# Performance work log

Measured on AMD Instinct MI355X. Metric: run time of the kernel, lower is better.

## Reference

```python
import jax, jax.numpy as jnp
import numpy as np

C = 768; NH = 12; HD = C // NH; P = 16; IMG = 256; HS = IMG // P  # 16x16 patch grid
WIN = 7; HWP = WIN // 2  # half window (pad)
DEPTH = 12; MLP = 4 * C
B = 32; T = 1
OFFS = [(dh, dw) for dh in range(WIN) for dw in range(WIN)]


def ln(x, g, b, eps=1e-5):
    mu = jnp.mean(x, axis=-1, keepdims=True)
    var = jnp.mean((x - mu) ** 2, axis=-1, keepdims=True)
    return (x - mu) * jax.lax.rsqrt(var + eps) * g + b


def local_attn(x, qkv_w, proj_w, proj_b):
    # x: (B, N, C) with N = HS*HS (T=1); sliding-window attention, zero-padded keys
    Bc, N, _ = x.shape
    qkv = (x @ qkv_w.T).reshape(Bc, N, 3, NH, HD)
    q, k, v = [jnp.transpose(qkv[:, :, i], (0, 2, 1, 3)).reshape(Bc, NH, HS, HS, HD)
               for i in range(3)]
    scale = HD ** -0.5
    kp = jnp.pad(k, ((0, 0), (0, 0), (HWP, HWP), (HWP, HWP), (0, 0)))
    vp = jnp.pad(v, ((0, 0), (0, 0), (HWP, HWP), (HWP, HWP), (0, 0)))
    # per-offset logits; padded (zero) keys give logit 0, matching torch's zero-pad softmax
    scores = jnp.stack([
        jnp.einsum('bnhwd,bnhwd->bnhw', q, kp[:, :, dh:dh + HS, dw:dw + HS]) * scale
        for dh, dw in OFFS], axis=-1)  # (B, NH, HS, HS, 49)
    attn = jax.nn.softmax(scores, axis=-1)
    out = sum(attn[..., i, None] * vp[:, :, dh:dh + HS, dw:dw + HS]
              for i, (dh, dw) in enumerate(OFFS))  # (B, NH, HS, HS, HD)
    out = jnp.transpose(out, (0, 2, 3, 1, 4)).reshape(Bc, N, C)
    return out @ proj_w.T + proj_b


def global_attn(x, in_w, in_b, out_w, out_b):
    Bc, N, _ = x.shape
    qkv = x @ in_w.T + in_b
    q, k, v = jnp.split(qkv, 3, axis=-1)
    hds = lambda t: t.reshape(Bc, N, NH, HD).transpose(0, 2, 1, 3)
    q, k, v = hds(q), hds(k), hds(v)
    s = jnp.einsum('bnqd,bnkd->bnqk', q, k) * (HD ** -0.5)
    a = jax.nn.softmax(s, axis=-1)
    o = jnp.einsum('bnqk,bnkd->bnqd', a, v).transpose(0, 2, 1, 3).reshape(Bc, N, C)
    return o @ out_w.T + out_b


def setup_inputs() -> dict:
    key = jax.random.key(0)
    ks = iter(jax.random.split(key, 40))
    s = 0.02
    inp = {
        'x': jax.random.normal(next(ks), (B, T, 3, IMG, IMG), jnp.float32),
        'aspect_ratio': jax.random.uniform(next(ks), (B,), jnp.float32),
        'conv_w': jax.random.normal(next(ks), (C, 3, P, P), jnp.float32) * s,
        'conv_b': jnp.zeros((C,), jnp.float32),
        'pe_g': jnp.ones((C,), jnp.float32), 'pe_b': jnp.zeros((C,), jnp.float32),
        'ar_token': jax.random.normal(next(ks), (1, 1, C), jnp.float32) * s,
        'pos_embed': jax.random.normal(next(ks), (1, 100 * HS * HS + 1, C), jnp.float32) * s,
        'ln1_g': jnp.ones((DEPTH, C), jnp.float32), 'ln1_b': jnp.zeros((DEPTH, C), jnp.float32),
        'ln2_g': jnp.ones((DEPTH, C), jnp.float32), 'ln2_b': jnp.zeros((DEPTH, C), jnp.float32),
        'loc_qkv_w': jax.random.normal(next(ks), (6, 3 * C, C), jnp.float32) * s,
        'loc_proj_w': jax.random.normal(next(ks), (6, C, C), jnp.float32) * s,
        'loc_proj_b': jnp.zeros((6, C), jnp.float32),
        'glob_in_w': jax.random.normal(next(ks), (6, 3 * C, C), jnp.float32) * s,
        'glob_in_b': jnp.zeros((6, 3 * C), jnp.float32),
        'glob_out_w': jax.random.normal(next(ks), (6, C, C), jnp.float32) * s,
        'glob_out_b': jnp.zeros((6, C), jnp.float32),
        'mlp_w1': jax.random.normal(next(ks), (DEPTH, MLP, C), jnp.float32) * s,
        'mlp_b1': jnp.zeros((DEPTH, MLP), jnp.float32),
        'mlp_w2': jax.random.normal(next(ks), (DEPTH, C, MLP), jnp.float32) * s,
        'mlp_b2': jnp.zeros((DEPTH, C), jnp.float32),
        'fin_g': jnp.ones((C,), jnp.float32), 'fin_b': jnp.zeros((C,), jnp.float32),
    }
    return inp


def reference(x, aspect_ratio, conv_w, conv_b, pe_g, pe_b, ar_token, pos_embed,
              ln1_g, ln1_b, ln2_g, ln2_b,
              loc_qkv_w, loc_proj_w, loc_proj_b,
              glob_in_w, glob_in_b, glob_out_w, glob_out_b,
              mlp_w1, mlp_b1, mlp_w2, mlp_b2, fin_g, fin_b):
    Bc, Tc, Ci, Hi, Wi = x.shape
    # patch embed: non-overlapping conv == block reshape + einsum
    xf = x.reshape(Bc * Tc, Ci, HS, P, HS, P)
    patches = jnp.einsum('bchpwq,ecpq->bhwe', xf, conv_w) + conv_b
    patches = patches.reshape(Bc, Tc * HS * HS, C)
    patches = ln(patches, pe_g, pe_b)
    # aspect ratio token
    ar = ar_token * (1.0 + aspect_ratio[:, None, None] * 0.1)  # (B,1,C)
    h = jnp.concatenate([patches, ar], axis=1)
    h = h + pos_embed[:, :h.shape[1], :]
    for i in range(DEPTH):
        if i % 2 == 0:  # local attention block (AR token stripped, N == HS*HS+1)
            li = i // 2
            tok, art = h[:, :-1], h[:, -1:]
            tok = tok + local_attn(ln(tok, ln1_g[i], ln1_b[i]),
                                   loc_qkv_w[li], loc_proj_w[li], loc_proj_b[li])
            h = jnp.concatenate([tok, art], axis=1)
        else:
            gi = i // 2
            h = h + global_attn(ln(h, ln1_g[i], ln1_b[i]),
                                glob_in_w[gi], glob_in_b[gi], glob_out_w[gi], glob_out_b[gi])
        m = ln(h, ln2_g[i], ln2_b[i])
        m = jax.nn.gelu(m @ mlp_w1[i].T + mlp_b1[i], approximate=False)
        h = h + m @ mlp_w2[i].T + mlp_b2[i]
    return ln(h, fin_g, fin_b)
```

## Files before the change

### kernel.cpp

```cpp
#include <hip/hip_runtime.h>
#include <cmath>

#define NHEADS 12
#define NTOK   257
#define BATCH  32
#define ROWS   (BATCH*NTOK)
#define PROWS  (BATCH*256)
#define GTPAD  288

typedef __attribute__((ext_vector_type(8))) short short8;
typedef __attribute__((ext_vector_type(8))) unsigned short u16x8;
typedef __attribute__((ext_vector_type(4))) float f32x4;

__device__ __forceinline__ unsigned short f2bf(float f) {
    unsigned u = __float_as_uint(f);
    unsigned r = (u + 0x7FFFu + ((u >> 16) & 1u)) >> 16;
    return (unsigned short)r;
}
__device__ __forceinline__ float b2f(unsigned short us) {
    return __uint_as_float((unsigned)us << 16);
}
__device__ __forceinline__ void gload16(const void* g, void* l) {
    __builtin_amdgcn_global_load_lds(
        (const __attribute__((address_space(1))) void*)g,
        (__attribute__((address_space(3))) void*)l, 16, 0, 0);
}

template<bool BIAS, bool GELU, bool RES, bool SKIPAR, bool OUTBF>
__global__ __launch_bounds__(256) void gemm_bf16(
    const unsigned short* __restrict__ A, const unsigned short* __restrict__ W,
    const float* __restrict__ bias, void* __restrict__ outv,
    int M, int N, int K)
{
    __shared__ unsigned short As[128 * 32];
    __shared__ unsigned short Bs[128 * 32];
    const int tid = threadIdx.x;
    const int lane = tid & 63, wid = tid >> 6;
    const int wr = wid >> 1, wc = wid & 1;
    const int bm = blockIdx.y * 128, bn = blockIdx.x * 128;

    f32x4 acc[4][4];
    #pragma unroll
    for (int i = 0; i < 4; i++)
        #pragma unroll
        for (int j = 0; j < 4; j++) acc[i][j] = (f32x4)0.f;

    const int srow = lane >> 2;
    const int skk  = (lane & 3) * 8;
    const int l15  = lane & 15;
    const int lg   = lane >> 4;

    for (int k0 = 0; k0 < K; k0 += 32) {
        #pragma unroll
        for (int cc = 0; cc < 2; cc++) {
            int c = 2 * wid + cc;
            int row = c * 16 + srow;
            gload16(A + (size_t)(bm + row) * K + k0 + skk, &As[c * 512]);
            gload16(W + (size_t)(bn + row) * K + k0 + skk, &Bs[c * 512]);
        }
        __syncthreads();
        short8 af[4], bf[4];
        #pragma unroll
        for (int i = 0; i < 4; i++)
            af[i] = *(const short8*)&As[(wr * 64 + i * 16 + l15) * 32 + lg * 8];
        #pragma unroll
        for (int j = 0; j < 4; j++)
            bf[j] = *(const short8*)&Bs[(wc * 64 + j * 16 + l15) * 32 + lg * 8];
        #pragma unroll
        for (int i = 0; i < 4; i++)
            #pragma unroll
            for (int j = 0; j < 4; j++)
                acc[i][j] = __builtin_amdgcn_mfma_f32_16x16x32_bf16(af[i], bf[j], acc[i][j], 0, 0, 0);
        __syncthreads();
    }

    float bcol[4];
    #pragma unroll
    for (int j = 0; j < 4; j++)
        bcol[j] = BIAS ? bias[bn + wc * 64 + j * 16 + l15] : 0.f;

    #pragma unroll
    for (int i = 0; i < 4; i++) {
        #pragma unroll
        for (int r = 0; r < 4; r++) {
            int row = bm + wr * 64 + i * 16 + lg * 4 + r;
            if (row >= M) continue;
            if (SKIPAR && (row % NTOK) == (NTOK - 1)) continue;
            #pragma unroll
            for (int j = 0; j < 4; j++) {
                int col = bn + wc * 64 + j * 16 + l15;
                float v = acc[i][j][r] + bcol[j];
                if (GELU) v = 0.5f * v * (1.0f + erff(v * 0.70710678118654752f));
                size_t idx = (size_t)row * N + col;
                if (OUTBF) {
                    ((unsigned short*)outv)[idx] = f2bf(v);
                } else {
                    float* o = (float*)outv;
                    if (RES) o[idx] += v; else o[idx] = v;
                }
            }
        }
    }
}

template<bool OUTBF>
__global__ __launch_bounds__(256) void ln_kernel(
    const float* __restrict__ in, void* __restrict__ outv,
    const float* __restrict__ g, const float* __restrict__ bparm, int rows)
{
    int gw = blockIdx.x * 4 + (threadIdx.x >> 6);
    int lane = threadIdx.x & 63;
    if (gw >= rows) return;
    const float* x = in + (size_t)gw * 768;
    float4 v[3];
    #pragma unroll
    for (int i = 0; i < 3; i++) v[i] = *(const float4*)(x + i * 256 + lane * 4);
    float s = 0.f;
    #pragma unroll
    for (int i = 0; i < 3; i++) s += v[i].x + v[i].y + v[i].z + v[i].w;
    #pragma unroll
    for (int off = 32; off >= 1; off >>= 1) s += __shfl_xor(s, off, 64);
    float mu = s * (1.f / 768.f);
    float q = 0.f;
    #pragma unroll
    for (int i = 0; i < 3; i++) {
        float dx = v[i].x - mu, dy = v[i].y - mu, dz = v[i].z - mu, dw = v[i].w - mu;
        q += dx * dx + dy * dy + dz * dz + dw * dw;
    }
    #pragma unroll
    for (int off = 32; off >= 1; off >>= 1) q += __shfl_xor(q, off, 64);
    float rstd = rsqrtf(q * (1.f / 768.f) + 1e-5f);
    #pragma unroll
    for (int i = 0; i < 3; i++) {
        float4 gg = *(const float4*)(g + i * 256 + lane * 4);
        float4 bb = *(const float4*)(bparm + i * 256 + lane * 4);
        float rx = (v[i].x - mu) * rstd * gg.x + bb.x;
        float ry = (v[i].y - mu) * rstd * gg.y + bb.y;
        float rz = (v[i].z - mu) * rstd * gg.z + bb.z;
        float rw = (v[i].w - mu) * rstd * gg.w + bb.w;
        if (OUTBF) {
            ushort4 u;
            u.x = f2bf(rx); u.y = f2bf(ry); u.z = f2bf(rz); u.w = f2bf(rw);
            *(ushort4*)((unsigned short*)outv + (size_t)gw * 768 + i * 256 + lane * 4) = u;
        } else {
            *(float4*)((float*)outv + (size_t)gw * 768 + i * 256 + lane * 4) =
                make_float4(rx, ry, rz, rw);
        }
    }
}

__global__ __launch_bounds__(256) void f2b_kernel(
    const float* __restrict__ in, unsigned short* __restrict__ out, int n4)
{
    int i = blockIdx.x * 256 + threadIdx.x;
    if (i >= n4) return;
    float4 v = ((const float4*)in)[i];
    ushort4 u;
    u.x = f2bf(v.x); u.y = f2bf(v.y); u.z = f2bf(v.z); u.w = f2bf(v.w);
    ((ushort4*)out)[i] = u;
}

__global__ __launch_bounds__(256) void gather_patches(
    const float* __restrict__ x, unsigned short* __restrict__ A)
{
    int row = blockIdx.x;
    int b = row >> 8;
    int pp = row & 255;
    int ph = pp >> 4, pw = pp & 15;
    const float* xb = x + (size_t)b * 196608;
    for (int e = threadIdx.x; e < 768; e += 256) {
        int c = e >> 8;
        int r = e & 255;
        int p = r >> 4, q = r & 15;
        A[(size_t)row * 768 + e] = f2bf(xb[(size_t)c * 65536 + (ph * 16 + p) * 256 + pw * 16 + q]);
    }
}

__global__ __launch_bounds__(256) void build_h_kernel(
    const unsigned short* __restrict__ lnp, const float* __restrict__ pos,
    const float* __restrict__ artok, const float* __restrict__ aspect,
    float* __restrict__ h)
{
    int row = blockIdx.x;
    int b = row / NTOK;
    int t = row - b * NTOK;
    float* hp = h + (size_t)row * 768;
    int e = threadIdx.x;
    if (t < 256) {
        const unsigned short* lp = lnp + ((size_t)b * 256 + t) * 768;
        const float* pp = pos + (size_t)t * 768;
        #pragma unroll
        for (int i = 0; i < 3; i++) { int c = e + i * 256; hp[c] = b2f(lp[c]) + pp[c]; }
    } else {
        float f = 1.0f + aspect[b] * 0.1f;
        const float* pp = pos + (size_t)256 * 768;
        #pragma unroll
        for (int i = 0; i < 3; i++) { int c = e + i * 256; hp[c] = artok[c] * f + pp[c]; }
    }
}

__global__ __launch_bounds__(256) void transpose_v(
    const unsigned short* __restrict__ qkv, unsigned short* __restrict__ vt)
{
    __shared__ unsigned short T[64][72];
    const int bh = blockIdx.x;
    const int b = bh / NHEADS, nh = bh % NHEADS;
    const unsigned short* vbase = qkv + (size_t)b * NTOK * 2304 + 1536 + nh * 64;
    unsigned short* obase = vt + (size_t)bh * 64 * GTPAD;
    const int tid = threadIdx.x;

    for (int t0 = 0; t0 < GTPAD; t0 += 64) {
        #pragma unroll
        for (int rnd = 0; rnd < 2; rnd++) {
            int tl = rnd * 32 + (tid >> 3);
            int d0 = (tid & 7) * 8;
            int tok = t0 + tl;
            u16x8 v;
            if (tok < NTOK) {
                v = *(const u16x8*)(vbase + (size_t)tok * 2304 + d0);
            } else {
                #pragma unroll
                for (int i = 0; i < 8; i++) v[i] = 0;
            }
            #pragma unroll
            for (int i = 0; i < 8; i++) T[d0 + i][tl] = v[i];
        }
        __syncthreads();
        int d = tid >> 2, ts = (tid & 3) * 16;
        if (t0 + ts < GTPAD) {
            u16x8 o0, o1;
            #pragma unroll
            for (int i = 0; i < 8; i++) { o0[i] = T[d][ts + i]; o1[i] = T[d][ts + 8 + i]; }
            *(u16x8*)(obase + (size_t)d * GTPAD + t0 + ts) = o0;
            *(u16x8*)(obase + (size_t)d * GTPAD + t0 + ts + 8) = o1;
        }
        __syncthreads();
    }
}

__global__ __launch_bounds__(256) void local_attn_mfma(
    const unsigned short* __restrict__ qkv, const unsigned short* __restrict__ vt,
    unsigned short* __restrict__ out)
{
    __shared__ unsigned short P[4][16 * 136];
    const int wid = threadIdx.x >> 6, lane = threadIdx.x & 63;
    const int gw = blockIdx.x * 4 + wid;
    const int bh = gw >> 4, h0 = gw & 15;
    const int b = bh / NHEADS, nh = bh % NHEADS;
    const int l15 = lane & 15, lg = lane >> 4;
    const unsigned short* base = qkv + (size_t)b * NTOK * 2304 + nh * 64;
    const unsigned short* vtb = vt + (size_t)bh * 64 * GTPAD;
    unsigned short* Pw = P[wid];

    const int qtok = h0 * 16 + l15;
    short8 qf0 = *(const short8*)(base + (size_t)qtok * 2304 + lg * 8);
    short8 qf1 = *(const short8*)(base + (size_t)qtok * 2304 + 32 + lg * 8);

    int r0 = h0 - 3; r0 = r0 < 0 ? 0 : (r0 > 8 ? 8 : r0);

    f32x4 s[8];
    #pragma unroll
    for (int i = 0; i < 8; i++) {
        const unsigned short* kr = base + (size_t)((r0 + i) * 16 + l15) * 2304 + 768;
        short8 kf0 = *(const short8*)(kr + lg * 8);
        short8 kf1 = *(const short8*)(kr + 32 + lg * 8);
        f32x4 z = (f32x4)0.f;
        z = __builtin_amdgcn_mfma_f32_16x16x32_bf16(kf0, qf0, z, 0, 0, 0);
        z = __builtin_amdgcn_mfma_f32_16x16x32_bf16(kf1, qf1, z, 0, 0, 0);
        s[i] = z;
    }

    const int vlo = l15 - 3 < 0 ? 0 : l15 - 3;
    const int vhi = l15 + 3 > 15 ? 15 : l15 + 3;
    const int rlo = h0 - 3 < 0 ? 0 : h0 - 3;
    const int rhi = h0 + 3 > 15 ? 15 : h0 + 3;
    const int n_oob = 49 - (rhi - rlo + 1) * (vhi - vlo + 1);
    float m = n_oob > 0 ? 0.f : -1e30f;
    float sv[32];
    #pragma unroll
    for (int i = 0; i < 8; i++) {
        int kh = r0 + i;
        bool rowok = (kh >= rlo) && (kh <= rhi);
        #pragma unroll
        for (int r = 0; r < 4; r++) {
            int kw = lg * 4 + r;
            bool ok = rowok && (kw >= vlo) && (kw <= vhi);
            float xx = ok ? s[i][r] * 0.125f : -1e30f;
            sv[i * 4 + r] = xx;
            m = fmaxf(m, xx);
        }
    }
    m = fmaxf(m, __shfl_xor(m, 16, 64));
    m = fmaxf(m, __shfl_xor(m, 32, 64));
    float tsum = 0.f;
    #pragma unroll
    for (int i = 0; i < 8; i++) {
        float p0 = __expf(sv[i * 4 + 0] - m);
        float p1 = __expf(sv[i * 4 + 1] - m);
        float p2 = __expf(sv[i * 4 + 2] - m);
        float p3 = __expf(sv[i * 4 + 3] - m);
        tsum += p0 + p1 + p2 + p3;
        unsigned u0 = (unsigned)f2bf(p0) | ((unsigned)f2bf(p1) << 16);
        unsigned u1 = (unsigned)f2bf(p2) | ((unsigned)f2bf(p3) << 16);
        *(uint2*)((char*)Pw + l15 * 272 + i * 32 + lg * 8) = make_uint2(u0, u1);
    }
    tsum += __shfl_xor(tsum, 16, 64);
    tsum += __shfl_xor(tsum, 32, 64);
    float denom = tsum + (float)n_oob * __expf(-m);
    __syncthreads();

    f32x4 acc[4];
    #pragma unroll
    for (int d = 0; d < 4; d++) acc[d] = (f32x4)0.f;
    #pragma unroll
    for (int kt = 0; kt < 128; kt += 32) {
        short8 pf = *(const short8*)((char*)Pw + l15 * 272 + kt * 2 + lg * 16);
        #pragma unroll
        for (int d = 0; d < 4; d++) {
            short8 vf = *(const short8*)(vtb + (size_t)(d * 16 + l15) * GTPAD + r0 * 16 + kt + lg * 8);
            acc[d] = __builtin_amdgcn_mfma_f32_16x16x32_bf16(vf, pf, acc[d], 0, 0, 0);
        }
    }

    float inv = 1.f / denom;
    unsigned short* op = out + ((size_t)b * NTOK + qtok) * 768 + nh * 64;
    #pragma unroll
    for (int d = 0; d < 4; d++) {
        ushort4 o;
        o.x = f2bf(acc[d][0] * inv);
        o.y = f2bf(acc[d][1] * inv);
        o.z = f2bf(acc[d][2] * inv);
        o.w = f2bf(acc[d][3] * inv);
        *(ushort4*)(op + d * 16 + lg * 4) = o;
    }
}

__global__ __launch_bounds__(64) void global_attn_mfma(
    const unsigned short* __restrict__ qkv, const unsigned short* __restrict__ vt,
    unsigned short* __restrict__ out)
{
    __shared__ uint4 Pbuf[80];
    unsigned short* P = (unsigned short*)Pbuf;
    const int blk = blockIdx.x;
    const int bh = blk / 17, qt = blk % 17;
    const int b = bh / NHEADS, nh = bh % NHEADS;
    const int lane = threadIdx.x;
    const int l15 = lane & 15, lg = lane >> 4;
    const unsigned short* base = qkv + (size_t)b * NTOK * 2304 + nh * 64;
    const unsigned short* vtb = vt + (size_t)bh * 64 * GTPAD;

    int qrow = qt * 16 + l15;
    const bool qvalid = qrow < NTOK;
    if (!qvalid) qrow = NTOK - 1;
    short8 qf[2];
    qf[0] = *(const short8*)(base + (size_t)qrow * 2304 + lg * 8);
    qf[1] = *(const short8*)(base + (size_t)qrow * 2304 + 32 + lg * 8);

    f32x4 acc[4];
    #pragma unroll
    for (int i = 0; i < 4; i++) acc[i] = (f32x4)0.f;
    float m = -1e30f, l = 0.f;

    for (int kt = 0; kt < GTPAD; kt += 32) {
        f32x4 s[2];
        #pragma unroll
        for (int hh = 0; hh < 2; hh++) {
            int krow = kt + hh * 16 + l15;
            if (krow > NTOK - 1) krow = NTOK - 1;
            short8 kf0 = *(const short8*)(base + (size_t)krow * 2304 + 768 + lg * 8);
            short8 kf1 = *(const short8*)(base + (size_t)krow * 2304 + 768 + 32 + lg * 8);
            f32x4 z = (f32x4)0.f;
            z = __builtin_amdgcn_mfma_f32_16x16x32_bf16(kf0, qf[0], z, 0, 0, 0);
            z = __builtin_amdgcn_mfma_f32_16x16x32_bf16(kf1, qf[1], z, 0, 0, 0);
            s[hh] = z;
        }
        float sv[8];
        float mt = -1e30f;
        #pragma unroll
        for (int hh = 0; hh < 2; hh++)
            #pragma unroll
            for (int r = 0; r < 4; r++) {
                int key = kt + hh * 16 + lg * 4 + r;
                float v = s[hh][r] * 0.125f;
                if (key >= NTOK) v = -1e30f;
                sv[hh * 4 + r] = v;
                mt = fmaxf(mt, v);
            }
        mt = fmaxf(mt, __shfl_xor(mt, 16, 64));
        mt = fmaxf(mt, __shfl_xor(mt, 32, 64));
        float mn = fmaxf(m, mt);
        float cf = __expf(m - mn);
        float tsum = 0.f;
        unsigned short pb[8];
        #pragma unroll
        for (int i = 0; i < 8; i++) {
            float p = __expf(sv[i] - mn);
            tsum += p;
            pb[i] = f2bf(p);
        }
        tsum += __shfl_xor(tsum, 16, 64);
        tsum += __shfl_xor(tsum, 32, 64);
        l = l * cf + tsum;
        m = mn;
        #pragma unroll
        for (int i = 0; i < 4; i++) acc[i] *= cf;

        unsigned u0 = (unsigned)pb[0] | ((unsigned)pb[1] << 16);
        unsigned u1 = (unsigned)pb[2] | ((unsigned)pb[3] << 16);
        unsigned u2 = (unsigned)pb[4] | ((unsigned)pb[5] << 16);
        unsigned u3 = (unsigned)pb[6] | ((unsigned)pb[7] << 16);
        *(uint2*)((char*)P + l15 * 80 + lg * 8)      = make_uint2(u0, u1);
        *(uint2*)((char*)P + l15 * 80 + 32 + lg * 8) = make_uint2(u2, u3);
        __syncthreads();
        short8 pf = *(const short8*)((char*)P + l15 * 80 + lg * 16);
        #pragma unroll
        for (int d = 0; d < 4; d++) {
            short8 vf = *(const short8*)(vtb + (size_t)(d * 16 + l15) * GTPAD + kt + lg * 8);
            acc[d] = __builtin_amdgcn_mfma_f32_16x16x32_bf16(vf, pf, acc[d], 0, 0, 0);
        }
        __syncthreads();
    }

    if (qvalid) {
        float inv = 1.f / l;
        unsigned short* op = out + ((size_t)b * NTOK + qrow) * 768 + nh * 64;
        #pragma unroll
        for (int d = 0; d < 4; d++) {
            ushort4 o;
            o.x = f2bf(acc[d][0] * inv);
            o.y = f2bf(acc[d][1] * inv);
            o.z = f2bf(acc[d][2] * inv);
            o.w = f2bf(acc[d][3] * inv);
            *(ushort4*)(op + d * 16 + lg * 4) = o;
        }
    }
}

extern "C" void kernel_launch(void* const* d_in, const int* in_sizes, int n_in,
                              void* d_out, int out_size, void* d_ws, size_t ws_size,
                              hipStream_t stream)
{
    const float* x       = (const float*)d_in[0];
    const float* aspect  = (const float*)d_in[1];
    const float* conv_w  = (const float*)d_in[2];
    const float* conv_b  = (const float*)d_in[3];
    const float* pe_g    = (const float*)d_in[4];
    const float* pe_b    = (const float*)d_in[5];
    const float* ar_tok  = (const float*)d_in[6];
    const float* pos     = (const float*)d_in[7];
    const float* ln1_g   = (const float*)d_in[8];
    const float* ln1_b   = (const float*)d_in[9];
    const float* ln2_g   = (const float*)d_in[10];
    const float* ln2_b   = (const float*)d_in[11];
    const float* loc_qkv_w  = (const float*)d_in[12];
    const float* loc_proj_w = (const float*)d_in[13];
    const float* loc_proj_b = (const float*)d_in[14];
    const float* glob_in_w  = (const float*)d_in[15];
    const float* glob_in_b  = (const float*)d_in[16];
    const float* glob_out_w = (const float*)d_in[17];
    const float* glob_out_b = (const float*)d_in[18];
    const float* mlp_w1  = (const float*)d_in[19];
    const float* mlp_b1  = (const float*)d_in[20];
    const float* mlp_w2  = (const float*)d_in[21];
    const float* mlp_b2  = (const float*)d_in[22];
    const float* fin_g   = (const float*)d_in[23];
    const float* fin_b   = (const float*)d_in[24];

    char* w = (char*)d_ws;
    float*          h     = (float*)w;
    unsigned short* lnb   = (unsigned short*)(w + 25264128);
    unsigned short* qkvb  = (unsigned short*)(w + 37896192);
    unsigned short* attnb = (unsigned short*)(w + 75792384);
    unsigned short* mlpb  = (unsigned short*)(w + 88424448);
    float*          pembf = (float*)mlpb;
    unsigned short* vtb   = mlpb;
    char* wp = w + 138952704;
    unsigned short* wconv  = (unsigned short*)wp;               wp += 1179648;
    unsigned short* wlqkv  = (unsigned short*)wp;               wp += 21233664;
    unsigned short* wlproj = (unsigned short*)wp;               wp += 7077888;
    unsigned short* wgin   = (unsigned short*)wp;               wp += 21233664;
    unsigned short* wgout  = (unsigned short*)wp;               wp += 7077888;
    unsigned short* wm1    = (unsigned short*)wp;               wp += 56623104;
    unsigned short* wm2    = (unsigned short*)wp;               wp += 56623104;

    auto cvt = [&](const float* src, unsigned short* dst, int n) {
        int n4 = n / 4;
        f2b_kernel<<<(n4 + 255) / 256, 256, 0, stream>>>(src, dst, n4);
    };
    cvt(conv_w,     wconv,  768 * 768);
    cvt(loc_qkv_w,  wlqkv,  6 * 2304 * 768);
    cvt(loc_proj_w, wlproj, 6 * 768 * 768);
    cvt(glob_in_w,  wgin,   6 * 2304 * 768);
    cvt(glob_out_w, wgout,  6 * 768 * 768);
    cvt(mlp_w1,     wm1,    12 * 3072 * 768);
    cvt(mlp_w2,     wm2,    12 * 768 * 3072);

    gather_patches<<<PROWS, 256, 0, stream>>>(x, qkvb);
    gemm_bf16<true, false, false, false, false><<<dim3(6, 64), 256, 0, stream>>>(
        qkvb, wconv, conv_b, pembf, PROWS, 768, 768);
    ln_kernel<true><<<PROWS / 4, 256, 0, stream>>>(pembf, attnb, pe_g, pe_b, PROWS);
    build_h_kernel<<<ROWS, 256, 0, stream>>>(attnb, pos, ar_tok, aspect, h);

    const int mt = (ROWS + 127) / 128;
    for (int i = 0; i < 12; i++) {
        int half = i / 2;
        ln_kernel<true><<<(ROWS + 3) / 4, 256, 0, stream>>>(h, lnb, ln1_g + i * 768, ln1_b + i * 768, ROWS);
        if ((i & 1) == 0) {
            gemm_bf16<false, false, false, false, true><<<dim3(18, mt), 256, 0, stream>>>(
                lnb, wlqkv + (size_t)half * 2304 * 768, nullptr, qkvb, ROWS, 2304, 768);
            transpose_v<<<BATCH * NHEADS, 256, 0, stream>>>(qkvb, vtb);
            local_attn_mfma<<<BATCH * NHEADS * 16 / 4, 256, 0, stream>>>(qkvb, vtb, attnb);
            gemm_bf16<true, false, true, true, false><<<dim3(6, mt), 256, 0, stream>>>(
                attnb, wlproj + (size_t)half * 768 * 768, loc_proj_b + half * 768, h, ROWS, 768, 768);
        } else {
            gemm_bf16<true, false, false, false, true><<<dim3(18, mt), 256, 0, stream>>>(
                lnb, wgin + (size_t)half * 2304 * 768, glob_in_b + half * 2304, qkvb, ROWS, 2304, 768);
            transpose_v<<<BATCH * NHEADS, 256, 0, stream>>>(qkvb, vtb);
            global_attn_mfma<<<BATCH * NHEADS * 17, 64, 0, stream>>>(qkvb, vtb, attnb);
            gemm_bf16<true, false, true, false, false><<<dim3(6, mt), 256, 0, stream>>>(
                attnb, wgout + (size_t)half * 768 * 768, glob_out_b + half * 768, h, ROWS, 768, 768);
        }
        ln_kernel<true><<<(ROWS + 3) / 4, 256, 0, stream>>>(h, lnb, ln2_g + i * 768, ln2_b + i * 768, ROWS);
        gemm_bf16<true, true, false, false, true><<<dim3(24, mt), 256, 0, stream>>>(
            lnb, wm1 + (size_t)i * 3072 * 768, mlp_b1 + i * 3072, mlpb, ROWS, 3072, 768);
        gemm_bf16<true, false, true, false, false><<<dim3(6, mt), 256, 0, stream>>>(
            mlpb, wm2 + (size_t)i * 768 * 3072, mlp_b2 + i * 768, h, ROWS, 768, 3072);
    }
    ln_kernel<false><<<(ROWS + 3) / 4, 256, 0, stream>>>(h, (float*)d_out, fin_g, fin_b, ROWS);
}
```

Before: 3.985 ms.

## Double-buffer GEMM LDS tiles with K=64, XOR swizzle and XCD-aware block remap

```diff
diff --git a/kernel.cpp b/kernel.cpp
--- a/kernel.cpp
+++ b/kernel.cpp
@@ -32,12 +32,20 @@
     const float* __restrict__ bias, void* __restrict__ outv,
     int M, int N, int K)
 {
-    __shared__ unsigned short As[128 * 32];
-    __shared__ unsigned short Bs[128 * 32];
+    __shared__ unsigned short As[2][128 * 64];
+    __shared__ unsigned short Bs[2][128 * 64];
     const int tid = threadIdx.x;
     const int lane = tid & 63, wid = tid >> 6;
     const int wr = wid >> 1, wc = wid & 1;
-    const int bm = blockIdx.y * 128, bn = blockIdx.x * 128;
+
+    const int gx = gridDim.x;
+    const int nwg = gx * gridDim.y;
+    const int orig = blockIdx.y * gx + blockIdx.x;
+    const int q8 = nwg >> 3, r8 = nwg & 7;
+    const int xcd = orig & 7, lid = orig >> 3;
+    const int wg = (xcd < r8 ? xcd * (q8 + 1) : r8 * (q8 + 1) + (xcd - r8) * q8) + lid;
+    const int bn = (wg % gx) * 128;
+    const int bm = (wg / gx) * 128;
 
     f32x4 acc[4][4];
     #pragma unroll
@@ -45,33 +53,49 @@
         #pragma unroll
         for (int j = 0; j < 4; j++) acc[i][j] = (f32x4)0.f;
 
-    const int srow = lane >> 2;
-    const int skk  = (lane & 3) * 8;
-    const int l15  = lane & 15;
-    const int lg   = lane >> 4;
-
-    for (int k0 = 0; k0 < K; k0 += 32) {
-        #pragma unroll
-        for (int cc = 0; cc < 2; cc++) {
-            int c = 2 * wid + cc;
-            int row = c * 16 + srow;
-            gload16(A + (size_t)(bm + row) * K + k0 + skk, &As[c * 512]);
-            gload16(W + (size_t)(bn + row) * K + k0 + skk, &Bs[c * 512]);
+    const int l15 = lane & 15;
+    const int lg  = lane >> 4;
+    const int sw  = l15 & 7;
+
+    auto stage = [&](int buf, int k0) {
+        #pragma unroll
+        for (int it = 0; it < 4; it++) {
+            int f = it * 256 + tid;
+            int row = f >> 3;
+            int g = (f & 7) ^ (row & 7);
+            gload16(A + (size_t)(bm + row) * K + k0 + g * 8, &As[buf][f * 8]);
+            gload16(W + (size_t)(bn + row) * K + k0 + g * 8, &Bs[buf][f * 8]);
+        }
+    };
+
+    const int nt = K >> 6;
+    stage(0, 0);
+    __syncthreads();
+
+    int buf = 0;
+    for (int t = 0; t < nt; t++) {
+        if (t + 1 < nt) stage(buf ^ 1, (t + 1) << 6);
+        #pragma unroll
+        for (int kk = 0; kk < 2; kk++) {
+            short8 af[4], bf[4];
+            #pragma unroll
+            for (int i = 0; i < 4; i++) {
+                int row = wr * 64 + i * 16 + l15;
+                af[i] = *(const short8*)&As[buf][row * 64 + (((kk * 4 + lg) ^ sw)) * 8];
+            }
+            #pragma unroll
+            for (int j = 0; j < 4; j++) {
+                int row = wc * 64 + j * 16 + l15;
+                bf[j] = *(const short8*)&Bs[buf][row * 64 + (((kk * 4 + lg) ^ sw)) * 8];
+            }
+            #pragma unroll
+            for (int i = 0; i < 4; i++)
+                #pragma unroll
+                for (int j = 0; j < 4; j++)
+                    acc[i][j] = __builtin_amdgcn_mfma_f32_16x16x32_bf16(af[i], bf[j], acc[i][j], 0, 0, 0);
         }
         __syncthreads();
-        short8 af[4], bf[4];
-        #pragma unroll
-        for (int i = 0; i < 4; i++)
-            af[i] = *(const short8*)&As[(wr * 64 + i * 16 + l15) * 32 + lg * 8];
-        #pragma unroll
-        for (int j = 0; j < 4; j++)
-            bf[j] = *(const short8*)&Bs[(wc * 64 + j * 16 + l15) * 32 + lg * 8];
-        #pragma unroll
-        for (int i = 0; i < 4; i++)
-            #pragma unroll
-            for (int j = 0; j < 4; j++)
-                acc[i][j] = __builtin_amdgcn_mfma_f32_16x16x32_bf16(af[i], bf[j], acc[i][j], 0, 0, 0);
-        __syncthreads();
+        buf ^= 1;
     }
 
     float bcol[4];
```

After: 3.682 ms. 7.6% less time.
